# Optimization experiments

Measured on AMD Instinct MI355X. Metric: run time of the kernel, lower is better.

The kernel has to match this reference:

```python
import jax, jax.numpy as jnp
from jax import lax
import numpy as np

H = 64  # LSTM_HIDDEN


def _lstm_layer(x, Wih, Whh, bih, bhh):
    """PyTorch-convention LSTM layer. x: [B,T,D]; Wih: [4H,D]; Whh: [4H,H]. Gate order i,f,g,o."""
    B = x.shape[0]
    h0 = jnp.zeros((B, H), x.dtype)
    c0 = jnp.zeros((B, H), x.dtype)
    # Precompute input contribution for all timesteps: [T,B,4H]
    xg = jnp.einsum('btd,gd->tbg', x, Wih) + bih + bhh

    def step(carry, xg_t):
        h, c = carry
        gates = xg_t + h @ Whh.T  # [B,4H]
        i, f, g, o = jnp.split(gates, 4, axis=-1)
        i = jax.nn.sigmoid(i)
        f = jax.nn.sigmoid(f)
        g = jnp.tanh(g)
        o = jax.nn.sigmoid(o)
        c = f * c + i * g
        h = o * jnp.tanh(c)
        return (h, c), h

    _, hs = lax.scan(step, (h0, c0), xg)  # hs: [T,B,H]
    return jnp.transpose(hs, (1, 0, 2))  # [B,T,H]


def setup_inputs() -> dict:
    key = jax.random.key(0)
    ks = jax.random.split(key, 12)
    B, T = 1024, 2048
    s = 1.0 / np.sqrt(H)  # PyTorch default uniform init bound
    u = lambda k, shape: jax.random.uniform(k, shape, jnp.float32, -s, s)
    return {
        'x': jax.random.normal(ks[0], (B, T), jnp.float32),
        'Wih0': u(ks[1], (4 * H, 1)),
        'Whh0': u(ks[2], (4 * H, H)),
        'bih0': u(ks[3], (4 * H,)),
        'bhh0': u(ks[4], (4 * H,)),
        'Wih1': u(ks[5], (4 * H, H)),
        'Whh1': u(ks[6], (4 * H, H)),
        'bih1': u(ks[7], (4 * H,)),
        'bhh1': u(ks[8], (4 * H,)),
        'fcW': u(ks[9], (1, H)),
        'fcb': u(ks[10], (1,)),
    }


def reference(x, Wih0, Whh0, bih0, bhh0, Wih1, Whh1, bih1, bhh1, fcW, fcb):
    x = x[..., None]  # unsqueeze(-1) -> [B,T,1]
    h1 = _lstm_layer(x, Wih0, Whh0, bih0, bhh0)   # [B,T,H]
    h2 = _lstm_layer(h1, Wih1, Whh1, bih1, bhh1)  # [B,T,H]
    last = h2[:, -1, :]                            # [B,H]
    logits = last @ fcW.T + fcb                    # [B,1]
    return jnp.squeeze(logits, axis=-1)            # [B]
```

## Files before the change

### kernel.cpp

```cpp
#include <hip/hip_runtime.h>

#define TT 2048
#define HD 64

#define H1_BASE 0
#define H2_BASE 1296
#define FCS_BASE 2576
#define PSTR 640
#define RSTR 160

#define SIC -1.4426950408889634f
#define SGC -2.8853900817779268f

#if __has_builtin(__builtin_amdgcn_exp2f)
#define EXP2F(x) __builtin_amdgcn_exp2f(x)
#else
#define EXP2F(x) __expf(0.69314718055994531f * (x))
#endif
#if __has_builtin(__builtin_amdgcn_rcpf)
#define RCPF(x) __builtin_amdgcn_rcpf(x)
#else
#define RCPF(x) (1.0f / (x))
#endif

__device__ __forceinline__ float rcp1p(float t) { return RCPF(1.0f + EXP2F(t)); }

typedef _Float16 v2h __attribute__((ext_vector_type(2)));

#if __has_builtin(__builtin_amdgcn_fdot2)
#define FDOT2(a, b, c) __builtin_amdgcn_fdot2((a), (b), (c), false)
#else
#define FDOT2(a, b, c) __fmaf_rn((float)(a)[1], (float)(b)[1], __fmaf_rn((float)(a)[0], (float)(b)[0], (c)))
#endif

static __device__ __forceinline__ v2h bch(float f) { return __builtin_bit_cast(v2h, f); }
static __device__ __forceinline__ v2h packw(float a, float b, float s) {
    v2h r; r[0] = (_Float16)(a * s); r[1] = (_Float16)(b * s); return r;
}

template<int CTRL>
__device__ __forceinline__ float dpp_get(float v) {
    return __int_as_float(__builtin_amdgcn_update_dpp(0, __float_as_int(v), CTRL, 0xF, 0xF, true));
}

#define BARRIER() asm volatile("s_waitcnt lgkmcnt(0)\n\ts_barrier" ::: "memory")

#define GDOT8I(acc, W) \
    acc = FDOT2(W##0, h0_, 0.0f); \
    acc = FDOT2(W##1, h1_, acc);  \
    acc = FDOT2(W##2, h2_, acc);  \
    acc = FDOT2(W##3, h3_, acc);  \
    acc = FDOT2(W##4, h4_, acc);  \
    acc = FDOT2(W##5, h5_, acc);  \
    acc = FDOT2(W##6, h6_, acc);  \
    acc = FDOT2(W##7, h7_, acc);

#define ROWDOTH(P, ROFF, A0, A1, A2, A3) { \
    const float4 f0_ = *(const float4*)(P##0 + (ROFF)); \
    const float4 f1_ = *(const float4*)(P##1 + (ROFF)); \
    const v2h h0_ = bch(f0_.x), h1_ = bch(f0_.y), h2_ = bch(f0_.z), h3_ = bch(f0_.w); \
    const v2h h4_ = bch(f1_.x), h5_ = bch(f1_.y), h6_ = bch(f1_.z), h7_ = bch(f1_.w); \
    GDOT8I(A0, wA) \
    GDOT8I(A1, wB) \
    GDOT8I(A2, wC) \
    GDOT8I(A3, wD) }

#define QRED(e, r0, r1, r2, r3) \
    float e; { \
        float x_ = q1 ? (r1) : (r0); float y_ = q1 ? (r0) : (r1); \
        x_ += dpp_get<0xB1>(y_); \
        float z_ = q1 ? (r3) : (r2); float w_ = q1 ? (r2) : (r3); \
        z_ += dpp_get<0xB1>(w_); \
        float u_ = q2 ? z_ : x_; float v_ = q2 ? x_ : z_; \
        e = u_ + dpp_get<0x4E>(v_); \
    }

#define STEP(P, X, L0WOFF, L1WOFF, DO_L1, XNI)                                  \
{                                                                               \
    float xv = 0.f;                                                             \
    if (isL0) {                                                                 \
        xv = X;                                                                 \
        const int xi_ = (XNI) < TT ? (XNI) : (TT - 1);                          \
        X = xps[xi_];                                                           \
    }                                                                           \
    float a00, a01, a02, a03, a10, a11, a12, a13;                               \
    float a20, a21, a22, a23, a30, a31, a32, a33;                               \
    ROWDOTH(P, 0 * RSTR, a00, a01, a02, a03)                                    \
    ROWDOTH(P, 1 * RSTR, a10, a11, a12, a13)                                    \
    ROWDOTH(P, 2 * RSTR, a20, a21, a22, a23)                                    \
    ROWDOTH(P, 3 * RSTR, a30, a31, a32, a33)                                    \
    QRED(e0_, a00, a10, a20, a30)                                               \
    QRED(e1_, a01, a11, a21, a31)                                               \
    QRED(e2_, a02, a12, a22, a32)                                               \
    QRED(e3_, a03, a13, a23, a33)                                               \
    if (isL0) {                                                                 \
        const float iv = rcp1p(__fmaf_rn(xv, wxm0, bgm0) + e0_);                \
        const float fv = rcp1p(__fmaf_rn(xv, wxm1, bgm1) + e1_);                \
        const float gv = __fmaf_rn(2.f, rcp1p(__fmaf_rn(xv, wxm2, bgm2) + e2_), -1.f); \
        const float ov = rcp1p(__fmaf_rn(xv, wxm3, bgm3) + e3_);                \
        cc = __fmaf_rn(fv, cc, iv * gv);                                        \
        const float th = __fmaf_rn(2.f, rcp1p(cc * SGC), -1.f);                 \
        *(_Float16*)(wraddr + (L0WOFF)) = (_Float16)(ov * th);                  \
    } else {                                                                    \
                   \
        e0_ += dpp_get<0x12C>(e0_);                                             \
        e1_ += dpp_get<0x12C>(e1_);                                             \
        e2_ += dpp_get<0x12C>(e2_);                                             \
        e3_ += dpp_get<0x12C>(e3_);                                             \
        if ((DO_L1) && ck < 4) {                                                \
            const float iv = rcp1p(e0_ + bgm0);                                 \
            const float fv = rcp1p(e1_ + bgm1);                                 \
            const float gv = __fmaf_rn(2.f, rcp1p(e2_ + bgm2), -1.f);           \
            const float ov = rcp1p(e3_ + bgm3);                                 \
            cc = __fmaf_rn(fv, cc, iv * gv);                                    \
            hlast = ov * __fmaf_rn(2.f, rcp1p(cc * SGC), -1.f);                 \
            *(_Float16*)(wraddr + (L1WOFF)) = (_Float16)hlast;                  \
        }                                                                       \
    }                                                                           \
    BARRIER();                                                                  \
}

__global__ __launch_bounds__(768, 3)
void lstm2_kernel(const float* __restrict__ x,
                  const float* __restrict__ Wih0,
                  const float* __restrict__ Whh0,
                  const float* __restrict__ bih0,
                  const float* __restrict__ bhh0,
                  const float* __restrict__ Wih1,
                  const float* __restrict__ Whh1,
                  const float* __restrict__ bih1,
                  const float* __restrict__ bhh1,
                  const float* __restrict__ fcW,
                  const float* __restrict__ fcb,
                  float* __restrict__ out)
{
    __shared__ __align__(16) float arena_f[912];
    char* const arena = (char*)arena_f;

    const int tid  = threadIdx.x;
    const int row0 = blockIdx.x * 4;

    const bool isL0 = (tid < 256);
    const int  p    = isL0 ? tid : (tid - 256);
    const int  j    = isL0 ? (p >> 2) : (p >> 3);
    const int  ck   = isL0 ? (p & 3)  : (p & 7);
    const int  ckk  = (ck < 4) ? ck : (ck - 4);
    const int  rk   = ck & 3;
    const bool q1   = (rk & 1) != 0;
    const bool q2   = (rk & 2) != 0;

    const float* Wsrc;
    if (isL0)        Wsrc = Whh0;
    else if (ck < 4) Wsrc = Wih1;
    else             Wsrc = Whh1;
    const int kbase = 16 * ckk;
    const float* Wg0 = Wsrc + (0 * HD + j) * HD + kbase;
    const float* Wg1 = Wsrc + (1 * HD + j) * HD + kbase;
    const float* Wg2 = Wsrc + (2 * HD + j) * HD + kbase;
    const float* Wg3 = Wsrc + (3 * HD + j) * HD + kbase;
    const v2h wA0 = packw(Wg0[0],  Wg0[1],  SIC), wA1 = packw(Wg0[2],  Wg0[3],  SIC),
              wA2 = packw(Wg0[4],  Wg0[5],  SIC), wA3 = packw(Wg0[6],  Wg0[7],  SIC),
              wA4 = packw(Wg0[8],  Wg0[9],  SIC), wA5 = packw(Wg0[10], Wg0[11], SIC),
              wA6 = packw(Wg0[12], Wg0[13], SIC), wA7 = packw(Wg0[14], Wg0[15], SIC);
    const v2h wB0 = packw(Wg1[0],  Wg1[1],  SIC), wB1 = packw(Wg1[2],  Wg1[3],  SIC),
              wB2 = packw(Wg1[4],  Wg1[5],  SIC), wB3 = packw(Wg1[6],  Wg1[7],  SIC),
              wB4 = packw(Wg1[8],  Wg1[9],  SIC), wB5 = packw(Wg1[10], Wg1[11], SIC),
              wB6 = packw(Wg1[12], Wg1[13], SIC), wB7 = packw(Wg1[14], Wg1[15], SIC);
    const v2h wC0 = packw(Wg2[0],  Wg2[1],  SGC), wC1 = packw(Wg2[2],  Wg2[3],  SGC),
              wC2 = packw(Wg2[4],  Wg2[5],  SGC), wC3 = packw(Wg2[6],  Wg2[7],  SGC),
              wC4 = packw(Wg2[8],  Wg2[9],  SGC), wC5 = packw(Wg2[10], Wg2[11], SGC),
              wC6 = packw(Wg2[12], Wg2[13], SGC), wC7 = packw(Wg2[14], Wg2[15], SGC);
    const v2h wD0 = packw(Wg3[0],  Wg3[1],  SIC), wD1 = packw(Wg3[2],  Wg3[3],  SIC),
              wD2 = packw(Wg3[4],  Wg3[5],  SIC), wD3 = packw(Wg3[6],  Wg3[7],  SIC),
              wD4 = packw(Wg3[8],  Wg3[9],  SIC), wD5 = packw(Wg3[10], Wg3[11], SIC),
              wD6 = packw(Wg3[12], Wg3[13], SIC), wD7 = packw(Wg3[14], Wg3[15], SIC);

    float bgm0, bgm1, bgm2, bgm3, wxm0 = 0.f, wxm1 = 0.f, wxm2 = 0.f, wxm3 = 0.f;
    if (isL0) {
        bgm0 = (bih0[0*HD+j] + bhh0[0*HD+j]) * SIC;
        bgm1 = (bih0[1*HD+j] + bhh0[1*HD+j]) * SIC;
        bgm2 = (bih0[2*HD+j] + bhh0[2*HD+j]) * SGC;
        bgm3 = (bih0[3*HD+j] + bhh0[3*HD+j]) * SIC;
        wxm0 = Wih0[0*HD+j] * SIC;
        wxm1 = Wih0[1*HD+j] * SIC;
        wxm2 = Wih0[2*HD+j] * SGC;
        wxm3 = Wih0[3*HD+j] * SIC;
    } else {
        bgm0 = (bih1[0*HD+j] + bhh1[0*HD+j]) * SIC;
        bgm1 = (bih1[1*HD+j] + bhh1[1*HD+j]) * SIC;
        bgm2 = (bih1[2*HD+j] + bhh1[2*HD+j]) * SGC;
        bgm3 = (bih1[3*HD+j] + bhh1[3*HD+j]) * SIC;
    }

    const int rdBase = (ck < 4) ? H1_BASE : H2_BASE;
    const int rdPh   = (ck < 4) ? 1 : 0;
    const int coff   = ckk * 32;

    const char* pe0 = arena + rdBase + rdPh * PSTR + coff;
    const char* pe1 = pe0 + 16;
    const char* po0 = arena + rdBase + (rdPh ^ 1) * PSTR + coff;
    const char* po1 = po0 + 16;

    char* const wraddr = arena + (isL0 ? H1_BASE : H2_BASE) + rk * RSTR + (j << 1);

    for (int z = tid; z < 644; z += 768)
        *(float*)(arena + 4 * z) = 0.f;

    const float* xps = x + (row0 + rk) * TT;
    float xa = 0.f, xb = 0.f;
    if (isL0) { xa = xps[0]; xb = xps[1]; }

    const float fcwj = fcW[j];
    float cc = 0.f, hlast = 0.f;

    __syncthreads();

    STEP(pe, xa, 0, PSTR, false, 2)
    STEP(po, xb, PSTR, 0, true, 3)
#pragma unroll 1
    for (int i = 2; i < TT; i += 2) {
        STEP(pe, xa, 0, PSTR, true, i + 2)
        STEP(po, xb, PSTR, 0, true, i + 3)
    }
    if (!isL0) {
        float a00, a01, a02, a03, a10, a11, a12, a13;
        float a20, a21, a22, a23, a30, a31, a32, a33;
        ROWDOTH(pe, 0 * RSTR, a00, a01, a02, a03)
        ROWDOTH(pe, 1 * RSTR, a10, a11, a12, a13)
        ROWDOTH(pe, 2 * RSTR, a20, a21, a22, a23)
        ROWDOTH(pe, 3 * RSTR, a30, a31, a32, a33)
        QRED(e0_, a00, a10, a20, a30)
        QRED(e1_, a01, a11, a21, a31)
        QRED(e2_, a02, a12, a22, a32)
        QRED(e3_, a03, a13, a23, a33)
        e0_ += dpp_get<0x12C>(e0_);
        e1_ += dpp_get<0x12C>(e1_);
        e2_ += dpp_get<0x12C>(e2_);
        e3_ += dpp_get<0x12C>(e3_);
        if (ck < 4) {
            const float iv = rcp1p(e0_ + bgm0);
            const float fv = rcp1p(e1_ + bgm1);
            const float gv = __fmaf_rn(2.f, rcp1p(e2_ + bgm2), -1.f);
            const float ov = rcp1p(e3_ + bgm3);
            cc = __fmaf_rn(fv, cc, iv * gv);
            hlast = ov * __fmaf_rn(2.f, rcp1p(cc * SGC), -1.f);
        }
    }
    __syncthreads();

    if (!isL0 && ck < 4)
        *(float*)(arena + FCS_BASE + ((rk * HD + j) << 2)) = hlast * fcwj;
    __syncthreads();

    if (tid < 64) {
        const int r = tid >> 4, seg = tid & 15;
        const float4 v = ((const float4*)(arena + FCS_BASE))[r * 16 + seg];
        float s = (v.x + v.y) + (v.z + v.w);
        s += __shfl_xor(s, 1, 64);
        s += __shfl_xor(s, 2, 64);
        s += __shfl_xor(s, 4, 64);
        s += __shfl_xor(s, 8, 64);
        if (seg == 0) out[row0 + r] = s + fcb[0];
    }
}

extern "C" void kernel_launch(void* const* d_in, const int* in_sizes, int n_in,
                              void* d_out, int out_size, void* d_ws, size_t ws_size,
                              hipStream_t stream) {
    const float* x    = (const float*)d_in[0];
    const float* Wih0 = (const float*)d_in[1];
    const float* Whh0 = (const float*)d_in[2];
    const float* bih0 = (const float*)d_in[3];
    const float* bhh0 = (const float*)d_in[4];
    const float* Wih1 = (const float*)d_in[5];
    const float* Whh1 = (const float*)d_in[6];
    const float* bih1 = (const float*)d_in[7];
    const float* bhh1 = (const float*)d_in[8];
    const float* fcW  = (const float*)d_in[9];
    const float* fcb  = (const float*)d_in[10];
    float* out = (float*)d_out;

    lstm2_kernel<<<256, 768, 0, stream>>>(x, Wih0, Whh0, bih0, bhh0,
                                          Wih1, Whh1, bih1, bhh1,
                                          fcW, fcb, out);
}
```

Measured before the change: 2.778 ms.

## Process two batch rows per block and launch twice as many blocks

Each block now handles 2 batch rows instead of 4, halving the per-step dot products and shrinking the reduction from a 4-way to a 2-way DPP exchange. Grid size doubles to 512 blocks so more CUs/SIMDs work in parallel on the serial recurrence. Shared memory shrinks accordingly and launch bounds now ask for 6 blocks per CU. Half of the lanes in each quad do redundant dot work, and register pressure under the tighter launch bound may cause spills.

```diff
diff --git a/kernel.cpp b/kernel.cpp
--- a/kernel.cpp
+++ b/kernel.cpp
@@ -4,9 +4,9 @@
 #define HD 64
 
 #define H1_BASE 0
-#define H2_BASE 1296
-#define FCS_BASE 2576
-#define PSTR 640
+#define H2_BASE 656
+#define FCS_BASE 1296
+#define PSTR 320
 #define RSTR 160
 
 #define SIC -1.4426950408889634f
@@ -65,14 +65,12 @@
     GDOT8I(A2, wC) \
     GDOT8I(A3, wD) }
 
-#define QRED(e, r0, r1, r2, r3) \
+#define QRED2(e, r0, r1) \
     float e; { \
-        float x_ = q1 ? (r1) : (r0); float y_ = q1 ? (r0) : (r1); \
+        float x_ = rr1 ? (r1) : (r0); \
+        float y_ = rr1 ? (r0) : (r1); \
         x_ += dpp_get<0xB1>(y_); \
-        float z_ = q1 ? (r3) : (r2); float w_ = q1 ? (r2) : (r3); \
-        z_ += dpp_get<0xB1>(w_); \
-        float u_ = q2 ? z_ : x_; float v_ = q2 ? x_ : z_; \
-        e = u_ + dpp_get<0x4E>(v_); \
+        e = x_ + dpp_get<0x4E>(x_); \
     }
 
 #define STEP(P, X, L0WOFF, L1WOFF, DO_L1, XNI)                                  \
@@ -84,30 +82,29 @@
         X = xps[xi_];                                                           \
     }                                                                           \
     float a00, a01, a02, a03, a10, a11, a12, a13;                               \
-    float a20, a21, a22, a23, a30, a31, a32, a33;                               \
     ROWDOTH(P, 0 * RSTR, a00, a01, a02, a03)                                    \
     ROWDOTH(P, 1 * RSTR, a10, a11, a12, a13)                                    \
-    ROWDOTH(P, 2 * RSTR, a20, a21, a22, a23)                                    \
-    ROWDOTH(P, 3 * RSTR, a30, a31, a32, a33)                                    \
-    QRED(e0_, a00, a10, a20, a30)                                               \
-    QRED(e1_, a01, a11, a21, a31)                                               \
-    QRED(e2_, a02, a12, a22, a32)                                               \
-    QRED(e3_, a03, a13, a23, a33)                                               \
+    QRED2(e0_, a00, a10)                                                        \
+    QRED2(e1_, a01, a11)                                                        \
+    QRED2(e2_, a02, a12)                                                        \
+    QRED2(e3_, a03, a13)                                                        \
     if (isL0) {                                                                 \
-        const float iv = rcp1p(__fmaf_rn(xv, wxm0, bgm0) + e0_);                \
-        const float fv = rcp1p(__fmaf_rn(xv, wxm1, bgm1) + e1_);                \
-        const float gv = __fmaf_rn(2.f, rcp1p(__fmaf_rn(xv, wxm2, bgm2) + e2_), -1.f); \
-        const float ov = rcp1p(__fmaf_rn(xv, wxm3, bgm3) + e3_);                \
-        cc = __fmaf_rn(fv, cc, iv * gv);                                        \
-        const float th = __fmaf_rn(2.f, rcp1p(cc * SGC), -1.f);                 \
-        *(_Float16*)(wraddr + (L0WOFF)) = (_Float16)(ov * th);                  \
+        if (rk < 2) {                                                           \
+            const float iv = rcp1p(__fmaf_rn(xv, wxm0, bgm0) + e0_);            \
+            const float fv = rcp1p(__fmaf_rn(xv, wxm1, bgm1) + e1_);            \
+            const float gv = __fmaf_rn(2.f, rcp1p(__fmaf_rn(xv, wxm2, bgm2) + e2_), -1.f); \
+            const float ov = rcp1p(__fmaf_rn(xv, wxm3, bgm3) + e3_);            \
+            cc = __fmaf_rn(fv, cc, iv * gv);                                    \
+            const float th = __fmaf_rn(2.f, rcp1p(cc * SGC), -1.f);             \
+            *(_Float16*)(wraddr + (L0WOFF)) = (_Float16)(ov * th);              \
+        }                                                                       \
     } else {                                                                    \
-                   \
+             \
         e0_ += dpp_get<0x12C>(e0_);                                             \
         e1_ += dpp_get<0x12C>(e1_);                                             \
         e2_ += dpp_get<0x12C>(e2_);                                             \
         e3_ += dpp_get<0x12C>(e3_);                                             \
-        if ((DO_L1) && ck < 4) {                                                \
+        if ((DO_L1) && ck < 2) {                                                \
             const float iv = rcp1p(e0_ + bgm0);                                 \
             const float fv = rcp1p(e1_ + bgm1);                                 \
             const float gv = __fmaf_rn(2.f, rcp1p(e2_ + bgm2), -1.f);           \
@@ -120,7 +117,7 @@
     BARRIER();                                                                  \
 }
 
-__global__ __launch_bounds__(768, 3)
+__global__ __launch_bounds__(768, 6)
 void lstm2_kernel(const float* __restrict__ x,
                   const float* __restrict__ Wih0,
                   const float* __restrict__ Whh0,
@@ -134,11 +131,11 @@
                   const float* __restrict__ fcb,
                   float* __restrict__ out)
 {
-    __shared__ __align__(16) float arena_f[912];
+    __shared__ __align__(16) float arena_f[452];
     char* const arena = (char*)arena_f;
 
     const int tid  = threadIdx.x;
-    const int row0 = blockIdx.x * 4;
+    const int row0 = blockIdx.x * 2;
 
     const bool isL0 = (tid < 256);
     const int  p    = isL0 ? tid : (tid - 256);
@@ -146,8 +143,7 @@
     const int  ck   = isL0 ? (p & 3)  : (p & 7);
     const int  ckk  = (ck < 4) ? ck : (ck - 4);
     const int  rk   = ck & 3;
-    const bool q1   = (rk & 1) != 0;
-    const bool q2   = (rk & 2) != 0;
+    const bool rr1  = (rk & 1) != 0;
 
     const float* Wsrc;
     if (isL0)        Wsrc = Whh0;
@@ -201,12 +197,12 @@
     const char* po0 = arena + rdBase + (rdPh ^ 1) * PSTR + coff;
     const char* po1 = po0 + 16;
 
-    char* const wraddr = arena + (isL0 ? H1_BASE : H2_BASE) + rk * RSTR + (j << 1);
-
-    for (int z = tid; z < 644; z += 768)
+    char* const wraddr = arena + (isL0 ? H1_BASE : H2_BASE) + (rk & 1) * RSTR + (j << 1);
+
+    for (int z = tid; z < 324; z += 768)
         *(float*)(arena + 4 * z) = 0.f;
 
-    const float* xps = x + (row0 + rk) * TT;
+    const float* xps = x + (row0 + (rk & 1)) * TT;
     float xa = 0.f, xb = 0.f;
     if (isL0) { xa = xps[0]; xb = xps[1]; }
 
@@ -224,20 +220,17 @@
     }
     if (!isL0) {
         float a00, a01, a02, a03, a10, a11, a12, a13;
-        float a20, a21, a22, a23, a30, a31, a32, a33;
         ROWDOTH(pe, 0 * RSTR, a00, a01, a02, a03)
         ROWDOTH(pe, 1 * RSTR, a10, a11, a12, a13)
-        ROWDOTH(pe, 2 * RSTR, a20, a21, a22, a23)
-        ROWDOTH(pe, 3 * RSTR, a30, a31, a32, a33)
-        QRED(e0_, a00, a10, a20, a30)
-        QRED(e1_, a01, a11, a21, a31)
-        QRED(e2_, a02, a12, a22, a32)
-        QRED(e3_, a03, a13, a23, a33)
+        QRED2(e0_, a00, a10)
+        QRED2(e1_, a01, a11)
+        QRED2(e2_, a02, a12)
+        QRED2(e3_, a03, a13)
         e0_ += dpp_get<0x12C>(e0_);
         e1_ += dpp_get<0x12C>(e1_);
         e2_ += dpp_get<0x12C>(e2_);
         e3_ += dpp_get<0x12C>(e3_);
-        if (ck < 4) {
+        if (ck < 2) {
             const float iv = rcp1p(e0_ + bgm0);
             const float fv = rcp1p(e1_ + bgm1);
             const float gv = __fmaf_rn(2.f, rcp1p(e2_ + bgm2), -1.f);
@@ -248,11 +241,11 @@
     }
     __syncthreads();
 
-    if (!isL0 && ck < 4)
-        *(float*)(arena + FCS_BASE + ((rk * HD + j) << 2)) = hlast * fcwj;
+    if (!isL0 && ck < 2)
+        *(float*)(arena + FCS_BASE + ((ck * HD + j) << 2)) = hlast * fcwj;
     __syncthreads();
 
-    if (tid < 64) {
+    if (tid < 32) {
         const int r = tid >> 4, seg = tid & 15;
         const float4 v = ((const float4*)(arena + FCS_BASE))[r * 16 + seg];
         float s = (v.x + v.y) + (v.z + v.w);
@@ -280,7 +273,7 @@
     const float* fcb  = (const float*)d_in[10];
     float* out = (float*)d_out;
 
-    lstm2_kernel<<<256, 768, 0, stream>>>(x, Wih0, Whh0, bih0, bhh0,
+    lstm2_kernel<<<512, 768, 0, stream>>>(x, Wih0, Whh0, bih0, bhh0,
                                           Wih1, Whh1, bih1, bhh1,
                                           fcW, fcb, out);
 }
```

Measured after the change: 3.122 ms. 1.12x slower.
